# Performance work log

Measured on AMD Instinct MI355X. Metric: run time of the kernel, lower is better.

## Reference

```python
import jax, jax.numpy as jnp
import numpy as np

D = 2560
H = 64
HD = D // H  # 40
TE = 512
FF = 4 * D  # 10240
EPS = 1e-5


def _ln(x, eps=EPS):
    # fp32 layernorm, no affine
    x32 = x.astype(jnp.float32)
    mu = jnp.mean(x32, axis=-1, keepdims=True)
    var = jnp.var(x32, axis=-1, keepdims=True)
    return ((x32 - mu) * jax.lax.rsqrt(var + eps)).astype(x.dtype)


def _rope(x, cos, sin):
    # x: [B, H, S_img, HD]; cos/sin: [S_img, HD]
    half = x.shape[-1] // 2
    xr, xi = x[..., :half], x[..., half:]
    x_rot = jnp.concatenate([-xi, xr], axis=-1)
    c = cos[None, None]
    s = sin[None, None]
    return (x.astype(jnp.float32) * c + x_rot.astype(jnp.float32) * s).astype(x.dtype)


def setup_inputs() -> dict:
    key = jax.random.key(0)
    ks = jax.random.split(key, 20)
    f = jnp.float32
    inp = {
        "hidden_states": jax.random.normal(ks[0], (1, 1024, D), f),
        "encoder_hidden_states": jax.random.normal(ks[1], (1, 128, D), f),
        "time_embed": jax.random.normal(ks[2], (1, TE), f),
        "rope_cos": jax.random.uniform(ks[3], (1024, HD), f),
        "rope_sin": jax.random.uniform(ks[4], (1024, HD), f),
        # AdaLayerNormZero linear: time_embed_dim -> 12*D
        "ada_w": jax.random.normal(ks[5], (TE, 12 * D), f) * 0.02,
        "ada_b": jnp.zeros((12 * D,), f),
        # attention projections (stored [in, out])
        "wq": jax.random.normal(ks[6], (D, D), f) * 0.02,
        "bq": jnp.zeros((D,), f),
        "wk": jax.random.normal(ks[7], (D, D), f) * 0.02,
        "bk": jnp.zeros((D,), f),
        "wv": jax.random.normal(ks[8], (D, D), f) * 0.02,
        "bv": jnp.zeros((D,), f),
        "wo": jax.random.normal(ks[9], (D, D), f) * 0.02,
        "bo": jnp.zeros((D,), f),
        # feedforward (shared for img and context streams)
        "w1": jax.random.normal(ks[10], (D, FF), f) * 0.02,
        "b1": jnp.zeros((FF,), f),
        "w2": jax.random.normal(ks[11], (FF, D), f) * 0.02,
        "b2": jnp.zeros((D,), f),
    }
    return inp


def _block(hidden_states, encoder_hidden_states, time_embed, rope_cos, rope_sin,
           ada_w, ada_b, wq, bq, wk, bk, wv, bv, wo, bo, w1, b1, w2, b2):
    B, T, _ = encoder_hidden_states.shape

    # --- AdaLayerNormZero ---
    emb = time_embed @ ada_w + ada_b  # [B, 12*D]
    (shift_msa, c_shift_msa, scale_msa, c_scale_msa, gate_msa, c_gate_msa,
     shift_mlp, c_shift_mlp, scale_mlp, c_scale_mlp, gate_mlp, c_gate_mlp) = jnp.split(emb, 12, axis=1)
    u = lambda v: v[:, None, :]  # [B,1,D]

    norm_h = _ln(hidden_states) * (1 + u(scale_msa)) + u(shift_msa)
    norm_e = _ln(encoder_hidden_states) * (1 + u(c_scale_msa)) + u(c_shift_msa)

    # --- SelfAttention on concatenated [text, image] sequence ---
    x = jnp.concatenate([norm_e, norm_h], axis=1)  # [B,S,D]
    S = x.shape[1]
    def heads(y):
        return y.reshape(B, S, H, HD).transpose(0, 2, 1, 3)  # [B,H,S,HD]
    q = heads(x @ wq + bq)
    k = heads(x @ wk + bk)
    v = heads(x @ wv + bv)
    q = _ln(q)  # fp32 QK-norm over head_dim
    k = _ln(k)
    # partial RoPE on image tokens only
    q = q.at[:, :, T:, :].set(_rope(q[:, :, T:, :], rope_cos, rope_sin))
    k = k.at[:, :, T:, :].set(_rope(k[:, :, T:, :], rope_cos, rope_sin))

    scores = jnp.einsum('bhqd,bhkd->bhqk', q, k) / np.sqrt(HD).astype(np.float32)
    attn = jax.nn.softmax(scores, axis=-1)
    o = jnp.einsum('bhqk,bhkd->bhqd', attn, v)  # [B,H,S,HD]
    o = o.transpose(0, 2, 1, 3).reshape(B, S, D)
    o = o @ wo + bo
    attn_e, attn_h = o[:, :T], o[:, T:]

    # --- residual with attn gates ---
    hidden_states = hidden_states + attn_h * u(gate_msa)
    encoder_hidden_states = encoder_hidden_states + attn_e * u(c_gate_msa)

    # --- MLP with AdaLN modulation + gates ---
    nh = _ln(hidden_states) * (1 + u(scale_mlp)) + u(shift_mlp)
    ne = _ln(encoder_hidden_states) * (1 + u(c_scale_mlp)) + u(c_shift_mlp)
    ff = lambda y: jax.nn.gelu(y @ w1 + b1, approximate=True) @ w2 + b2
    hidden_states = hidden_states + ff(nh) * u(gate_mlp)
    encoder_hidden_states = encoder_hidden_states + ff(ne) * u(c_gate_mlp)
    return hidden_states, encoder_hidden_states


def reference(hidden_states, encoder_hidden_states, time_embed, rope_cos, rope_sin,
              ada_w, ada_b, wq, bq, wk, bk, wv, bv, wo, bo, w1, b1, w2, b2):
    return _block(hidden_states, encoder_hidden_states, time_embed, rope_cos, rope_sin,
                  ada_w, ada_b, wq, bq, wk, bk, wv, bv, wo, bo, w1, b1, w2, b2)
```

## Files before the change

kernel.cpp:

```cpp
#include <hip/hip_runtime.h>
#include <stdint.h>

#define D 2560
#define NH 64
#define HD 40
#define TE_ 512
#define FFD 10240
#define TENC 128
#define THID 1024
#define SEQ 1152

typedef __bf16 bf16_t;
typedef __bf16 bf16x8 __attribute__((ext_vector_type(8)));
typedef float  f32x4  __attribute__((ext_vector_type(4)));

__device__ __forceinline__ void gld_lds16(const void* g, void* l) {
  __builtin_amdgcn_global_load_lds((__attribute__((address_space(1))) void*)(g),
                                   (__attribute__((address_space(3))) void*)(l), 16, 0, 0);
}

__device__ __forceinline__ void wtrans_tile(const float* __restrict__ W, bf16_t* __restrict__ Wt,
                                            int K, int N, int bk, int bn, int tid,
                                            float* tile ) {
  #pragma unroll
  for (int i = 0; i < 4; ++i) {
    int c = i * 256 + tid;
    int r = c >> 4, q = c & 15;
    f32x4 v = *(const f32x4*)(W + (size_t)(bk * 64 + r) * N + bn * 64 + q * 4);
    tile[r * 65 + q * 4 + 0] = v[0]; tile[r * 65 + q * 4 + 1] = v[1];
    tile[r * 65 + q * 4 + 2] = v[2]; tile[r * 65 + q * 4 + 3] = v[3];
  }
  __syncthreads();
  #pragma unroll
  for (int i = 0; i < 2; ++i) {
    int c = i * 256 + tid;
    int n = c >> 3, kc = c & 7;
    bf16x8 o;
    #pragma unroll
    for (int j = 0; j < 8; ++j) o[j] = (bf16_t)tile[(kc * 8 + j) * 65 + n];
    *(bf16x8*)(Wt + (size_t)(bn * 64 + n) * K + bk * 64 + kc * 8) = o;
  }
}

__global__ __launch_bounds__(256) void prep1(
    const float* __restrict__ te, const float* __restrict__ aw, const float* __restrict__ ab,
    float* __restrict__ emb,
    const float* __restrict__ wq, const float* __restrict__ wk, const float* __restrict__ wv,
    bf16_t* __restrict__ wqkvT,
    const float* __restrict__ bq, const float* __restrict__ bk, const float* __restrict__ bv,
    float* __restrict__ bqkv, bf16_t* __restrict__ vt) {
  __shared__ float tile[64 * 65];
  const int b = blockIdx.x, t = threadIdx.x;
  if (b < 120) {
    int j = b * 256 + t;
    float acc = ab[j];
    #pragma unroll 8
    for (int k = 0; k < TE_; ++k) acc = fmaf(te[k], aw[(size_t)k * (12 * D) + j], acc);
    emb[j] = acc;
  } else if (b < 1720) {
    int l = b - 120;  wtrans_tile(wq, wqkvT,                     D, D, l % 40, l / 40, t, tile);
  } else if (b < 3320) {
    int l = b - 1720; wtrans_tile(wk, wqkvT + (size_t)D * D,     D, D, l % 40, l / 40, t, tile);
  } else if (b < 4920) {
    int l = b - 3320; wtrans_tile(wv, wqkvT + (size_t)2 * D * D, D, D, l % 40, l / 40, t, tile);
  } else if (b < 4950) {
    int i = (b - 4920) * 256 + t;
    bqkv[i] = i < D ? bq[i] : (i < 2 * D ? bk[i - D] : bv[i - 2 * D]);
  } else {
    int i = (b - 4950) * 256 + t;
    int h = i / 1152, g = i - h * 1152;
    bf16x8 z = {};
    if (g < 144) {
      #pragma unroll
      for (int j = 0; j < 8; ++j) z[j] = (bf16_t)1.f;
    }
    *(bf16x8*)(vt + ((size_t)h * 48 + 40) * SEQ + g * 8) = z;
  }
}

__global__ void ln_mod(const float* __restrict__ hid, const float* __restrict__ enc,
                       const float* __restrict__ emb, bf16_t* __restrict__ out,
                       int shift_h, int scale_h, int shift_e, int scale_e) {
  int row = blockIdx.x, tid = threadIdx.x;
  const float *src, *sc, *sh;
  if (row < TENC) { src = enc + (size_t)row * D;          sc = emb + scale_e * D; sh = emb + shift_e * D; }
  else            { src = hid + (size_t)(row - TENC) * D; sc = emb + scale_h * D; sh = emb + shift_h * D; }
  float v[10], s = 0.f, s2 = 0.f;
  #pragma unroll
  for (int i = 0; i < 10; ++i) { v[i] = src[tid + i * 256]; s += v[i]; s2 += v[i] * v[i]; }
  #pragma unroll
  for (int o = 32; o > 0; o >>= 1) { s += __shfl_down(s, o); s2 += __shfl_down(s2, o); }
  __shared__ float red[8];
  int wv = tid >> 6, ln = tid & 63;
  if (ln == 0) { red[wv] = s; red[4 + wv] = s2; }
  __syncthreads();
  s  = red[0] + red[1] + red[2] + red[3];
  s2 = red[4] + red[5] + red[6] + red[7];
  float mean = s * (1.f / D);
  float rstd = rsqrtf(s2 * (1.f / D) - mean * mean + 1e-5f);
  #pragma unroll
  for (int i = 0; i < 10; ++i) {
    int c = tid + i * 256;
    out[(size_t)row * D + c] = (bf16_t)((v[i] - mean) * rstd * (1.f + sc[c]) + sh[c]);
  }
}

template<int EPI>
__device__ __forceinline__ void gemm_body(
    bf16_t* As, bf16_t* Bs,
    const bf16_t* __restrict__ A, const bf16_t* __restrict__ Bt,
    const float* __restrict__ bias, int Kld, int ksteps, int N, int nM, int nMN,
    int nwg, int orig,
    bf16_t* __restrict__ outb, float* __restrict__ outp) {
  const int q8 = nwg >> 3, r8 = nwg & 7;
  const int xcd = orig & 7, pos = orig >> 3;
  const int wg = (xcd < r8 ? xcd * (q8 + 1) : r8 * (q8 + 1) + (xcd - r8) * q8) + pos;
  const int part = wg / nMN, rest = wg - part * nMN;
  const int bm = rest % nM, bn = rest / nM;
  const int m0 = bm * 128, n0 = bn * 128;
  const int kbase = part * ksteps;
  const int tid = threadIdx.x, wv = tid >> 6, ln = tid & 63;
  const int wr = wv >> 1, wc = wv & 1, lr = ln & 15, lg = ln >> 4;

  f32x4 acc[4][4];
  const f32x4 zero = {0.f, 0.f, 0.f, 0.f};
  #pragma unroll
  for (int m = 0; m < 4; ++m)
    #pragma unroll
    for (int n = 0; n < 4; ++n) acc[m][n] = zero;

  for (int t = 0; t < ksteps; ++t) {
    const int k0 = (kbase + t) << 6;
    __syncthreads();
    #pragma unroll
    for (int i = 0; i < 4; ++i) {
      int g = wv * 4 + i;
      int s = g * 64 + ln;
      int r = s >> 3, ks = s & 7;
      gld_lds16(A + (size_t)(m0 + r) * Kld + k0 + ((ks ^ (r & 7)) << 3), &As[g * 512]);
    }
    #pragma unroll
    for (int i = 0; i < 4; ++i) {
      int g = wv * 4 + i;
      int s = g * 64 + ln;
      int r = s >> 3, ks = s & 7;
      gld_lds16(Bt + (size_t)(n0 + r) * Kld + k0 + ((ks ^ (r & 7)) << 3), &Bs[g * 512]);
    }
    __syncthreads();
    #pragma unroll
    for (int ks2 = 0; ks2 < 2; ++ks2) {
      int ko = ks2 * 4 + lg;
      bf16x8 af[4], bfr[4];
      #pragma unroll
      for (int m = 0; m < 4; ++m) {
        int r = wr * 64 + m * 16 + lr;
        af[m] = *(const bf16x8*)&As[r * 64 + ((ko ^ (r & 7)) << 3)];
      }
      #pragma unroll
      for (int n = 0; n < 4; ++n) {
        int c = wc * 64 + n * 16 + lr;
        bfr[n] = *(const bf16x8*)&Bs[c * 64 + ((ko ^ (c & 7)) << 3)];
      }
      #pragma unroll
      for (int m = 0; m < 4; ++m)
        #pragma unroll
        for (int n = 0; n < 4; ++n)
          acc[m][n] = __builtin_amdgcn_mfma_f32_16x16x32_bf16(af[m], bfr[n], acc[m][n], 0, 0, 0);
    }
  }

  #pragma unroll
  for (int m = 0; m < 4; ++m) {
    int row = m0 + wr * 64 + m * 16 + (lg << 2);
    #pragma unroll
    for (int n = 0; n < 4; ++n) {
      int col = n0 + wc * 64 + n * 16 + lr;
      float bv = (EPI == 4) ? 0.f : bias[col];
      #pragma unroll
      for (int r = 0; r < 4; ++r) {
        float val = acc[m][n][r] + bv;
        int rr = row + r;
        if (EPI == 1) {
          float z = 0.7978845608028654f * (val + 0.044715f * val * val * val);
          float t2 = 1.f - 2.f / (__expf(2.f * z) + 1.f);
          outb[(size_t)rr * N + col] = (bf16_t)(0.5f * val * (1.f + t2));
        } else {
          outp[(size_t)part * SEQ * N + (size_t)rr * N + col] = val;
        }
      }
    }
  }
}

template<int EPI>
__global__ __launch_bounds__(256, 4) void gemm4(
    const bf16_t* __restrict__ A, const bf16_t* __restrict__ Bt,
    const float* __restrict__ bias, int Kld, int ksteps, int N, int nM, int nMN,
    bf16_t* __restrict__ outb, float* __restrict__ outp) {
  __shared__ bf16_t As[128 * 64];
  __shared__ bf16_t Bs[128 * 64];
  gemm_body<EPI>(As, Bs, A, Bt, bias, Kld, ksteps, N, nM, nMN, gridDim.x, blockIdx.x,
                 outb, outp);
}

__global__ __launch_bounds__(256, 4) void qkv_g(
    const bf16_t* __restrict__ A, const bf16_t* __restrict__ wqkvT,
    float* __restrict__ qparts,
    const float* __restrict__ wo, bf16_t* __restrict__ woT) {
  __shared__ char smem[32768] __attribute__((aligned(16)));
  const int b = blockIdx.x;
  if (b < 1080) {
    gemm_body<4>((bf16_t*)smem, (bf16_t*)(smem + 16384), A, wqkvT, nullptr,
                 D, 20, 3 * D, 9, 540, 1080, b, nullptr, qparts);
  } else {
    int l = b - 1080;
    wtrans_tile(wo, woT, D, D, l % 40, l / 40, threadIdx.x, (float*)smem);
  }
}

__global__ __launch_bounds__(256) void qkv_red(
    const float* __restrict__ parts, const float* __restrict__ bqkv,
    const float* __restrict__ rc, const float* __restrict__ rs,
    bf16_t* __restrict__ qb, bf16_t* __restrict__ kb, bf16_t* __restrict__ vt) {
  const int r = blockIdx.x, t = threadIdx.x;
  const int h = t >> 2, sub = t & 3;
  __shared__ float cs_s[HD], sn_s[HD];
  const bool rope = (r >= TENC);
  if (rope && t < 2 * HD) {
    if (t < HD) cs_s[t] = rc[(size_t)(r - TENC) * HD + t];
    else        sn_s[t - HD] = rs[(size_t)(r - TENC) * HD + (t - HD)];
  }
  const float* p0 = parts + (size_t)r * (3 * D);
  const float* p1 = p0 + (size_t)SEQ * (3 * D);
  const int cq = h * HD + sub * 10;
  float q[10], k[10], v[10];
  #pragma unroll
  for (int j = 0; j < 10; ++j) {
    q[j] = p0[cq + j] + p1[cq + j] + bqkv[cq + j];
    k[j] = p0[D + cq + j] + p1[D + cq + j] + bqkv[D + cq + j];
    v[j] = p0[2 * D + cq + j] + p1[2 * D + cq + j] + bqkv[2 * D + cq + j];
  }
  __syncthreads();
  float qs = 0.f, qs2 = 0.f, ks = 0.f, ks2 = 0.f;
  #pragma unroll
  for (int j = 0; j < 10; ++j) { qs += q[j]; qs2 += q[j] * q[j]; ks += k[j]; ks2 += k[j] * k[j]; }
  qs += __shfl_xor(qs, 1); qs += __shfl_xor(qs, 2);
  qs2 += __shfl_xor(qs2, 1); qs2 += __shfl_xor(qs2, 2);
  ks += __shfl_xor(ks, 1); ks += __shfl_xor(ks, 2);
  ks2 += __shfl_xor(ks2, 1); ks2 += __shfl_xor(ks2, 2);
  float qm = qs * (1.f / HD), km = ks * (1.f / HD);
  float qr = rsqrtf(qs2 * (1.f / HD) - qm * qm + 1e-5f);
  float kr = rsqrtf(ks2 * (1.f / HD) - km * km + 1e-5f);
  #pragma unroll
  for (int j = 0; j < 10; ++j) { q[j] = (q[j] - qm) * qr; k[j] = (k[j] - km) * kr; }
  if (rope) {
    float pq[10], pk[10];
    #pragma unroll
    for (int j = 0; j < 10; ++j) { pq[j] = __shfl_xor(q[j], 2); pk[j] = __shfl_xor(k[j], 2); }
    #pragma unroll
    for (int j = 0; j < 10; ++j) {
      int d = sub * 10 + j;
      float c = cs_s[d], s = sn_s[d];
      if (d < 20) { q[j] = q[j] * c - pq[j] * s; k[j] = k[j] * c - pk[j] * s; }
      else        { q[j] = q[j] * c + pq[j] * s; k[j] = k[j] * c + pk[j] * s; }
    }
  }
  bf16_t* qd = qb + ((size_t)h * SEQ + r) * 64;
  bf16_t* kd = kb + ((size_t)h * SEQ + r) * 64;
  const float qscale = 0.15811388300841897f;
  #pragma unroll
  for (int j = 0; j < 10; ++j) {
    int d = sub * 10 + j;
    qd[d] = (bf16_t)(q[j] * qscale);
    kd[d] = (bf16_t)k[j];
  }
  #pragma unroll
  for (int j = 0; j < 6; ++j) {
    int d = 40 + sub * 6 + j;
    qd[d] = (bf16_t)0.f; kd[d] = (bf16_t)0.f;
  }
  #pragma unroll
  for (int j = 0; j < 10; ++j) {
    int d = sub * 10 + j;
    vt[((size_t)h * 48 + d) * SEQ + r] = (bf16_t)v[j];
  }
}

template<int P>
__global__ void redk(const float* __restrict__ parts, const float* __restrict__ bias,
                     const float* __restrict__ emb, int gate_h, int gate_e,
                     const float* __restrict__ res_h, const float* __restrict__ res_e,
                     float* __restrict__ out_h, float* __restrict__ out_e) {
  int idx = blockIdx.x * 256 + threadIdx.x;
  int row = idx / (D / 4), col = (idx - row * (D / 4)) * 4;
  f32x4 s = *(const f32x4*)(bias + col);
  #pragma unroll
  for (int p = 0; p < P; ++p)
    s += *(const f32x4*)(parts + (size_t)p * SEQ * D + (size_t)row * D + col);
  const float* res; float* out; int g;
  int r2;
  if (row < TENC) { res = res_e; out = out_e; g = gate_e; r2 = row; }
  else            { res = res_h; out = out_h; g = gate_h; r2 = row - TENC; }
  f32x4 g4 = *(const f32x4*)(emb + (size_t)g * D + col);
  f32x4 rr4 = *(const f32x4*)(res + (size_t)r2 * D + col);
  f32x4 o;
  #pragma unroll
  for (int j = 0; j < 4; ++j) o[j] = rr4[j] + s[j] * g4[j];
  *(f32x4*)(out + (size_t)r2 * D + col) = o;
}

template<int P>
__global__ __launch_bounds__(256) void redk_ln(
    const float* __restrict__ parts, const float* __restrict__ bias,
    const float* __restrict__ emb, int gate_h, int gate_e,
    int shift_h, int scale_h, int shift_e, int scale_e,
    const float* __restrict__ res_h, const float* __restrict__ res_e,
    float* __restrict__ out_h, float* __restrict__ out_e, bf16_t* __restrict__ xout) {
  int row = blockIdx.x, tid = threadIdx.x;
  const float* res; float* out; int g, sh, sc; int r2;
  if (row < TENC) { res = res_e; out = out_e; g = gate_e; sh = shift_e; sc = scale_e; r2 = row; }
  else            { res = res_h; out = out_h; g = gate_h; sh = shift_h; sc = scale_h; r2 = row - TENC; }
  float v[10], s = 0.f, s2 = 0.f;
  #pragma unroll
  for (int i = 0; i < 10; ++i) {
    int c = tid + i * 256;
    float val = bias[c];
    #pragma unroll
    for (int p = 0; p < P; ++p) val += parts[(size_t)p * SEQ * D + (size_t)row * D + c];
    val = res[(size_t)r2 * D + c] + val * emb[(size_t)g * D + c];
    out[(size_t)r2 * D + c] = val;
    v[i] = val; s += val; s2 += val * val;
  }
  #pragma unroll
  for (int o = 32; o > 0; o >>= 1) { s += __shfl_down(s, o); s2 += __shfl_down(s2, o); }
  __shared__ float red[8];
  int wvv = tid >> 6, lnn = tid & 63;
  if (lnn == 0) { red[wvv] = s; red[4 + wvv] = s2; }
  __syncthreads();
  s  = red[0] + red[1] + red[2] + red[3];
  s2 = red[4] + red[5] + red[6] + red[7];
  float mean = s * (1.f / D);
  float rstd = rsqrtf(s2 * (1.f / D) - mean * mean + 1e-5f);
  #pragma unroll
  for (int i = 0; i < 10; ++i) {
    int c = tid + i * 256;
    xout[(size_t)row * D + c] =
        (bf16_t)((v[i] - mean) * rstd * (1.f + emb[(size_t)sc * D + c]) + emb[(size_t)sh * D + c]);
  }
}

__global__ __launch_bounds__(256) void attn_plus(
    const bf16_t* __restrict__ qb, const bf16_t* __restrict__ kb,
    const bf16_t* __restrict__ vt, bf16_t* __restrict__ obf,
    const float* __restrict__ w1, bf16_t* __restrict__ w1T,
    const float* __restrict__ w2, bf16_t* __restrict__ w2T) {
  __shared__ char smem[22528] __attribute__((aligned(16)));
  const int b = blockIdx.x;
  if (b >= 1152) {
    if (b < 7552) { int l = b - 1152; wtrans_tile(w1, w1T, D, FFD, l % 40, l / 40, threadIdx.x, (float*)smem); }
    else          { int l = b - 7552; wtrans_tile(w2, w2T, FFD, D, l % 160, l / 160, threadIdx.x, (float*)smem); }
    return;
  }
  bf16_t* Ks = (bf16_t*)smem;
  bf16_t* Vs = (bf16_t*)(smem + 8192);
  bf16_t* Ps = (bf16_t*)(smem + 14336);
  const int h = b & 63;
  const int qblk = b >> 6;
  const int tid = threadIdx.x, wv = tid >> 6, ln = tid & 63;
  const int qbase = qblk * 64 + wv * 16;
  const int lr = ln & 15, lg = ln >> 4;

  bf16x8 af[2];
  {
    const bf16_t* qp = qb + ((size_t)h * SEQ + qbase + lr) * 64 + lg * 8;
    af[0] = *(const bf16x8*)(qp);
    af[1] = *(const bf16x8*)(qp + 32);
  }
  const f32x4 zero = {0.f, 0.f, 0.f, 0.f};
  f32x4 acc[3];
  acc[0] = zero; acc[1] = zero; acc[2] = zero;

  const bf16_t* kbh = kb + (size_t)h * SEQ * 64;
  const bf16_t* vth = vt + (size_t)h * 48 * SEQ;

  for (int kv0 = 0; kv0 < SEQ; kv0 += 64) {
    __syncthreads();
    #pragma unroll
    for (int i = 0; i < 2; ++i) {
      int g = wv * 2 + i;
      int slot = g * 64 + ln;
      int kr = slot >> 3, so = slot & 7;
      gld_lds16(kbh + (size_t)(kv0 + kr) * 64 + ((so ^ (kr & 7)) << 3), &Ks[g * 512]);
    }
    #pragma unroll
    for (int i = 0; i < 2; ++i) {
      int g = wv + 4 * i;
      if (g < 6) {
        int slot = g * 64 + ln;
        int dr = slot >> 3, so = slot & 7;
        gld_lds16(vth + (size_t)dr * SEQ + kv0 + ((so ^ (dr & 7)) << 3), &Vs[g * 512]);
      }
    }
    __syncthreads();
    f32x4 s[4];
    #pragma unroll
    for (int nt = 0; nt < 4; ++nt) {
      s[nt] = zero;
      int kvr = nt * 16 + lr;
      #pragma unroll
      for (int kk = 0; kk < 2; ++kk) {
        bf16x8 bk = *(const bf16x8*)&Ks[kvr * 64 + (((kk * 4 + lg) ^ (kvr & 7)) << 3)];
        s[nt] = __builtin_amdgcn_mfma_f32_16x16x32_bf16(af[kk], bk, s[nt], 0, 0, 0);
      }
    }
    #pragma unroll
    for (int nt = 0; nt < 4; ++nt)
      #pragma unroll
      for (int r = 0; r < 4; ++r) {
        float p = exp2f(fmaf(s[nt][r], 1.44269504f, -9.377517766f));
        int q = lg * 4 + r;
        int kv = nt * 16 + lr;
        Ps[wv * 1024 + q * 64 + ((((kv >> 3) ^ (q & 7)) << 3) | (kv & 7))] = (bf16_t)p;
      }
    bf16x8 pa[2];
    #pragma unroll
    for (int kk = 0; kk < 2; ++kk)
      pa[kk] = *(const bf16x8*)&Ps[wv * 1024 + lr * 64 + (((kk * 4 + lg) ^ (lr & 7)) << 3)];
    #pragma unroll
    for (int dt = 0; dt < 3; ++dt) {
      #pragma unroll
      for (int kk = 0; kk < 2; ++kk) {
        int dr = dt * 16 + lr;
        bf16x8 bv = *(const bf16x8*)&Vs[dr * 64 + (((kk * 4 + lg) ^ (dr & 7)) << 3)];
        acc[dt] = __builtin_amdgcn_mfma_f32_16x16x32_bf16(pa[kk], bv, acc[dt], 0, 0, 0);
      }
    }
  }
  float linv[4];
  #pragma unroll
  for (int r = 0; r < 4; ++r)
    linv[r] = 1.f / __shfl(acc[2][r], (ln & 48) | 8);
  #pragma unroll
  for (int dt = 0; dt < 3; ++dt) {
    int d = dt * 16 + lr;
    if (d < HD) {
      #pragma unroll
      for (int r = 0; r < 4; ++r) {
        int q = qbase + lg * 4 + r;
        obf[(size_t)q * D + h * HD + d] = (bf16_t)(acc[dt][r] * linv[r]);
      }
    }
  }
}

extern "C" void kernel_launch(void* const* d_in, const int* in_sizes, int n_in,
                              void* d_out, int out_size, void* d_ws, size_t ws_size,
                              hipStream_t stream) {
  const float* hid = (const float*)d_in[0];
  const float* enc = (const float*)d_in[1];
  const float* tem = (const float*)d_in[2];
  const float* rc  = (const float*)d_in[3];
  const float* rs  = (const float*)d_in[4];
  const float* aw  = (const float*)d_in[5];
  const float* ab  = (const float*)d_in[6];
  const float* wq  = (const float*)d_in[7];
  const float* bq  = (const float*)d_in[8];
  const float* wk  = (const float*)d_in[9];
  const float* bk  = (const float*)d_in[10];
  const float* wvv = (const float*)d_in[11];
  const float* bv  = (const float*)d_in[12];
  const float* wo  = (const float*)d_in[13];
  const float* bo  = (const float*)d_in[14];
  const float* w1  = (const float*)d_in[15];
  const float* b1  = (const float*)d_in[16];
  const float* w2  = (const float*)d_in[17];
  const float* b2  = (const float*)d_in[18];
  float* out_hid = (float*)d_out;
  float* out_enc = out_hid + (size_t)THID * D;

  char* ws = (char*)d_ws;
  size_t off = 0;
  auto alloc = [&](size_t b) { char* p = ws + off; off += (b + 255) & ~(size_t)255; return p; };
  float*  emb  = (float*) alloc((size_t)12 * D * 4);
  bf16_t* xln  = (bf16_t*)alloc((size_t)SEQ * D * 2);
  bf16_t* aff  = (bf16_t*)alloc((size_t)SEQ * FFD * 2);
  bf16_t* vt   = (bf16_t*)alloc((size_t)NH * 48 * SEQ * 2);
  bf16_t* qbb  = (bf16_t*)alloc((size_t)NH * SEQ * 64 * 2);
  bf16_t* kbb  = (bf16_t*)alloc((size_t)NH * SEQ * 64 * 2);
  bf16_t* wqkvT= (bf16_t*)alloc((size_t)3 * D * D * 2);
  bf16_t* woT  = (bf16_t*)alloc((size_t)D * D * 2);
  bf16_t* w1T  = (bf16_t*)alloc((size_t)FFD * D * 2);
  bf16_t* w2T  = (bf16_t*)alloc((size_t)D * FFD * 2);
  float*  bqkv = (float*) alloc((size_t)3 * D * 4);
  bf16_t* obf = xln;
  float*  h1  = (float*)qbb;
  float*  e1  = h1 + (size_t)THID * D;
  float*  qparts = (float*)w1T;
  float*  oparts = (float*)wqkvT;
  float*  fparts = (float*)wqkvT;

  prep1<<<dim3(5238), dim3(256), 0, stream>>>(tem, aw, ab, emb, wq, wk, wvv,
      wqkvT, bq, bk, bv, bqkv, vt);
  ln_mod<<<dim3(SEQ), dim3(256), 0, stream>>>(hid, enc, emb, xln, 0, 2, 1, 3);
  qkv_g<<<dim3(2680), dim3(256), 0, stream>>>(xln, wqkvT, qparts, wo, woT);
  qkv_red<<<dim3(SEQ), dim3(256), 0, stream>>>(qparts, bqkv, rc, rs, qbb, kbb, vt);
  attn_plus<<<dim3(13952), dim3(256), 0, stream>>>(qbb, kbb, vt, obf, w1, w1T, w2, w2T);
  gemm4<4><<<dim3(360), dim3(256), 0, stream>>>(obf, woT, nullptr, D, 20, D, 9, 180,
      nullptr, oparts);
  redk_ln<2><<<dim3(SEQ), dim3(256), 0, stream>>>(oparts, bo, emb, 4, 5, 6, 8, 7, 9,
      hid, enc, h1, e1, xln);
  gemm4<1><<<dim3(720), dim3(256), 0, stream>>>(xln, w1T, b1, D, 40, FFD, 9, 720,
      aff, nullptr);
  gemm4<4><<<dim3(720), dim3(256), 0, stream>>>(aff, w2T, nullptr, FFD, 40, D, 9, 180,
      nullptr, fparts);
  redk<4><<<dim3(2880), dim3(256), 0, stream>>>(fparts, b2, emb, 10, 11, h1, e1, out_hid, out_enc);
}
```

Baseline: 462.1 us.

## Double attention query tile per wave and move w2 transpose into out-projection launch

Each attention block now handles 128 queries instead of 64, with every wave processing two 16-row query fragments that share the K and V fragments loaded from LDS. This halves the number of attention blocks and the redundant K/V global-to-LDS loads. The w2 weight transpose moves out of the attention launch and is packed alongside the output-projection GEMM in a new combined kernel, which balances the work across the two launches. The costs are higher register and LDS use per block and fewer attention blocks, which may lower occupancy.

```diff
diff --git a/kernel.cpp b/kernel.cpp
--- a/kernel.cpp
+++ b/kernel.cpp
@@ -218,6 +218,21 @@
   }
 }
 
+__global__ __launch_bounds__(256, 4) void oproj_plus(
+    const bf16_t* __restrict__ A, const bf16_t* __restrict__ woT,
+    float* __restrict__ oparts,
+    const float* __restrict__ w2, bf16_t* __restrict__ w2T) {
+  __shared__ char smem[32768] __attribute__((aligned(16)));
+  const int b = blockIdx.x;
+  if (b < 360) {
+    gemm_body<4>((bf16_t*)smem, (bf16_t*)(smem + 16384), A, woT, nullptr,
+                 D, 20, D, 9, 180, 360, b, nullptr, oparts);
+  } else {
+    int l = b - 360;
+    wtrans_tile(w2, w2T, FFD, D, l % 160, l / 160, threadIdx.x, (float*)smem);
+  }
+}
+
 __global__ __launch_bounds__(256) void qkv_red(
     const float* __restrict__ parts, const float* __restrict__ bqkv,
     const float* __restrict__ rc, const float* __restrict__ rs,
@@ -352,13 +367,12 @@
 __global__ __launch_bounds__(256) void attn_plus(
     const bf16_t* __restrict__ qb, const bf16_t* __restrict__ kb,
     const bf16_t* __restrict__ vt, bf16_t* __restrict__ obf,
-    const float* __restrict__ w1, bf16_t* __restrict__ w1T,
-    const float* __restrict__ w2, bf16_t* __restrict__ w2T) {
-  __shared__ char smem[22528] __attribute__((aligned(16)));
+    const float* __restrict__ w1, bf16_t* __restrict__ w1T) {
+  __shared__ char smem[30720] __attribute__((aligned(16)));
   const int b = blockIdx.x;
-  if (b >= 1152) {
-    if (b < 7552) { int l = b - 1152; wtrans_tile(w1, w1T, D, FFD, l % 40, l / 40, threadIdx.x, (float*)smem); }
-    else          { int l = b - 7552; wtrans_tile(w2, w2T, FFD, D, l % 160, l / 160, threadIdx.x, (float*)smem); }
+  if (b >= 576) {
+    int l = b - 576;
+    wtrans_tile(w1, w1T, D, FFD, l % 40, l / 40, threadIdx.x, (float*)smem);
     return;
   }
   bf16_t* Ks = (bf16_t*)smem;
@@ -367,18 +381,20 @@
   const int h = b & 63;
   const int qblk = b >> 6;
   const int tid = threadIdx.x, wv = tid >> 6, ln = tid & 63;
-  const int qbase = qblk * 64 + wv * 16;
+  const int qbase = qblk * 128 + wv * 32;
   const int lr = ln & 15, lg = ln >> 4;
 
-  bf16x8 af[2];
-  {
-    const bf16_t* qp = qb + ((size_t)h * SEQ + qbase + lr) * 64 + lg * 8;
-    af[0] = *(const bf16x8*)(qp);
-    af[1] = *(const bf16x8*)(qp + 32);
+  bf16x8 af[2][2];
+  #pragma unroll
+  for (int qf = 0; qf < 2; ++qf) {
+    const bf16_t* qp = qb + ((size_t)h * SEQ + qbase + qf * 16 + lr) * 64 + lg * 8;
+    af[qf][0] = *(const bf16x8*)(qp);
+    af[qf][1] = *(const bf16x8*)(qp + 32);
   }
   const f32x4 zero = {0.f, 0.f, 0.f, 0.f};
-  f32x4 acc[3];
-  acc[0] = zero; acc[1] = zero; acc[2] = zero;
+  f32x4 acc[2][3];
+  #pragma unroll
+  for (int qf = 0; qf < 2; ++qf) { acc[qf][0] = zero; acc[qf][1] = zero; acc[qf][2] = zero; }
 
   const bf16_t* kbh = kb + (size_t)h * SEQ * 64;
   const bf16_t* vth = vt + (size_t)h * 48 * SEQ;
@@ -402,52 +418,57 @@
       }
     }
     __syncthreads();
-    f32x4 s[4];
     #pragma unroll
     for (int nt = 0; nt < 4; ++nt) {
-      s[nt] = zero;
       int kvr = nt * 16 + lr;
+      bf16x8 bk0 = *(const bf16x8*)&Ks[kvr * 64 + ((lg ^ (kvr & 7)) << 3)];
+      bf16x8 bk1 = *(const bf16x8*)&Ks[kvr * 64 + (((4 + lg) ^ (kvr & 7)) << 3)];
+      #pragma unroll
+      for (int qf = 0; qf < 2; ++qf) {
+        f32x4 s = zero;
+        s = __builtin_amdgcn_mfma_f32_16x16x32_bf16(af[qf][0], bk0, s, 0, 0, 0);
+        s = __builtin_amdgcn_mfma_f32_16x16x32_bf16(af[qf][1], bk1, s, 0, 0, 0);
+        #pragma unroll
+        for (int r = 0; r < 4; ++r) {
+          float p = exp2f(fmaf(s[r], 1.44269504f, -9.377517766f));
+          int q = lg * 4 + r;
+          int kv = nt * 16 + lr;
+          Ps[(wv * 2 + qf) * 1024 + q * 64 + ((((kv >> 3) ^ (q & 7)) << 3) | (kv & 7))] = (bf16_t)p;
+        }
+      }
+    }
+    bf16x8 pa[2][2];
+    #pragma unroll
+    for (int qf = 0; qf < 2; ++qf)
+      #pragma unroll
+      for (int kk = 0; kk < 2; ++kk)
+        pa[qf][kk] = *(const bf16x8*)&Ps[(wv * 2 + qf) * 1024 + lr * 64 + (((kk * 4 + lg) ^ (lr & 7)) << 3)];
+    #pragma unroll
+    for (int dt = 0; dt < 3; ++dt) {
+      int dr = dt * 16 + lr;
       #pragma unroll
       for (int kk = 0; kk < 2; ++kk) {
-        bf16x8 bk = *(const bf16x8*)&Ks[kvr * 64 + (((kk * 4 + lg) ^ (kvr & 7)) << 3)];
-        s[nt] = __builtin_amdgcn_mfma_f32_16x16x32_bf16(af[kk], bk, s[nt], 0, 0, 0);
-      }
-    }
-    #pragma unroll
-    for (int nt = 0; nt < 4; ++nt)
-      #pragma unroll
-      for (int r = 0; r < 4; ++r) {
-        float p = exp2f(fmaf(s[nt][r], 1.44269504f, -9.377517766f));
-        int q = lg * 4 + r;
-        int kv = nt * 16 + lr;
-        Ps[wv * 1024 + q * 64 + ((((kv >> 3) ^ (q & 7)) << 3) | (kv & 7))] = (bf16_t)p;
-      }
-    bf16x8 pa[2];
-    #pragma unroll
-    for (int kk = 0; kk < 2; ++kk)
-      pa[kk] = *(const bf16x8*)&Ps[wv * 1024 + lr * 64 + (((kk * 4 + lg) ^ (lr & 7)) << 3)];
+        bf16x8 bv = *(const bf16x8*)&Vs[dr * 64 + (((kk * 4 + lg) ^ (dr & 7)) << 3)];
+        acc[0][dt] = __builtin_amdgcn_mfma_f32_16x16x32_bf16(pa[0][kk], bv, acc[0][dt], 0, 0, 0);
+        acc[1][dt] = __builtin_amdgcn_mfma_f32_16x16x32_bf16(pa[1][kk], bv, acc[1][dt], 0, 0, 0);
+      }
+    }
+  }
+  #pragma unroll
+  for (int qf = 0; qf < 2; ++qf) {
+    float linv[4];
+    #pragma unroll
+    for (int r = 0; r < 4; ++r)
+      linv[r] = 1.f / __shfl(acc[qf][2][r], (ln & 48) | 8);
     #pragma unroll
     for (int dt = 0; dt < 3; ++dt) {
-      #pragma unroll
-      for (int kk = 0; kk < 2; ++kk) {
-        int dr = dt * 16 + lr;
-        bf16x8 bv = *(const bf16x8*)&Vs[dr * 64 + (((kk * 4 + lg) ^ (dr & 7)) << 3)];
-        acc[dt] = __builtin_amdgcn_mfma_f32_16x16x32_bf16(pa[kk], bv, acc[dt], 0, 0, 0);
-      }
-    }
-  }
-  float linv[4];
-  #pragma unroll
-  for (int r = 0; r < 4; ++r)
-    linv[r] = 1.f / __shfl(acc[2][r], (ln & 48) | 8);
-  #pragma unroll
-  for (int dt = 0; dt < 3; ++dt) {
-    int d = dt * 16 + lr;
-    if (d < HD) {
-      #pragma unroll
-      for (int r = 0; r < 4; ++r) {
-        int q = qbase + lg * 4 + r;
-        obf[(size_t)q * D + h * HD + d] = (bf16_t)(acc[dt][r] * linv[r]);
+      int d = dt * 16 + lr;
+      if (d < HD) {
+        #pragma unroll
+        for (int r = 0; r < 4; ++r) {
+          int q = qbase + qf * 16 + lg * 4 + r;
+          obf[(size_t)q * D + h * HD + d] = (bf16_t)(acc[qf][dt][r] * linv[r]);
+        }
       }
     }
   }
@@ -504,9 +525,8 @@
   ln_mod<<<dim3(SEQ), dim3(256), 0, stream>>>(hid, enc, emb, xln, 0, 2, 1, 3);
   qkv_g<<<dim3(2680), dim3(256), 0, stream>>>(xln, wqkvT, qparts, wo, woT);
   qkv_red<<<dim3(SEQ), dim3(256), 0, stream>>>(qparts, bqkv, rc, rs, qbb, kbb, vt);
-  attn_plus<<<dim3(13952), dim3(256), 0, stream>>>(qbb, kbb, vt, obf, w1, w1T, w2, w2T);
-  gemm4<4><<<dim3(360), dim3(256), 0, stream>>>(obf, woT, nullptr, D, 20, D, 9, 180,
-      nullptr, oparts);
+  attn_plus<<<dim3(6976), dim3(256), 0, stream>>>(qbb, kbb, vt, obf, w1, w1T);
+  oproj_plus<<<dim3(6760), dim3(256), 0, stream>>>(obf, woT, oparts, w2, w2T);
   redk_ln<2><<<dim3(SEQ), dim3(256), 0, stream>>>(oparts, bo, emb, 4, 5, 6, 8, 7, 9,
       hid, enc, h1, e1, xln);
   gemm4<1><<<dim3(720), dim3(256), 0, stream>>>(xln, w1T, b1, D, 40, FFD, 9, 720,
```

Result: faster. 442.2 us (-4.3%).
